# Optimization experiments

Hardware: AMD Instinct MI355X
Metric: run time of the kernel (lower is better)

The kernel has to match this reference:

```python
import jax, jax.numpy as jnp
import numpy as np

T_IN, T_OUT = 16, 25          # in_length, out_length
B, K = 4096, 32               # heroes, neighbors per hero
N = B * K                     # total neighbor tracks
ENC, DEC, DYN, EMB = 64, 128, 32, 32


def _lrelu(x):
    return jnp.where(x >= 0, x, 0.1 * x)


def _lstm(x, Wih, Whh, bih, bhh, hidden):
    """PyTorch-convention LSTM (gate order i,f,g,o). x: [T, B, D]. Returns (all_h [T,B,H], last_h [B,H])."""
    z = jnp.zeros((x.shape[1], hidden), x.dtype)

    def step(carry, xt):
        h, c = carry
        g = xt @ Wih.T + bih + h @ Whh.T + bhh
        i, f, gg, o = jnp.split(g, 4, axis=-1)
        c = jax.nn.sigmoid(f) * c + jax.nn.sigmoid(i) * jnp.tanh(gg)
        h = jax.nn.sigmoid(o) * jnp.tanh(c)
        return (h, c), h

    (h, c), hs = jax.lax.scan(step, (z, z), x)
    return hs, h


def setup_inputs() -> dict:
    key = jax.random.key(0)
    ks = jax.random.split(key, 20)
    p = lambda k, s: jax.random.normal(k, s, jnp.float32) * 0.1
    return {
        "hist": jax.random.normal(ks[0], (T_IN, B, 2), jnp.float32),
        "nbrs": jax.random.normal(ks[1], (T_IN, N, 2), jnp.float32),
        "Wip": p(ks[2], (EMB, 2)), "bip": p(ks[3], (EMB,)),
        "Wih_e": p(ks[4], (4 * ENC, EMB)), "Whh_e": p(ks[5], (4 * ENC, ENC)),
        "bih_e": p(ks[6], (4 * ENC,)), "bhh_e": p(ks[7], (4 * ENC,)),
        "Wdyn": p(ks[8], (DYN, ENC)), "bdyn": p(ks[9], (DYN,)),
        "Wnbr": p(ks[10], (ENC, 2 * T_IN)), "bnbr": p(ks[11], (ENC,)),
        "Wih_d": p(ks[12], (4 * DEC, 2 * DYN)), "Whh_d": p(ks[13], (4 * DEC, DEC)),
        "bih_d": p(ks[14], (4 * DEC,)), "bhh_d": p(ks[15], (4 * DEC,)),
        "Wop": p(ks[16], (2, DEC)), "bop": p(ks[17], (2,)),
        # index_division flattened: neighbor j belongs to hero segment_ids[j] (sorted, K per hero)
        "segment_ids": jnp.repeat(jnp.arange(B, dtype=jnp.int32), K),
    }


def reference(hist, nbrs, Wip, bip, Wih_e, Whh_e, bih_e, bhh_e, Wdyn, bdyn,
              Wnbr, bnbr, Wih_d, Whh_d, bih_d, bhh_d, Wop, bop, segment_ids):
    # --- encode ego history ---
    emb = _lrelu(hist @ Wip.T + bip)                       # [T,B,EMB]
    _, h_enc = _lstm(emb, Wih_e, Whh_e, bih_e, bhh_e, ENC)  # [B,ENC]
    hist_e = _lrelu(h_enc @ Wdyn.T + bdyn)                 # [B,DYN]

    # --- relative neighbor tracks + ragged segment-max pooling ---
    relative = hist[:, segment_ids, :] - nbrs              # [T,N,2]  (hero_repeated gather)
    rela = jnp.transpose(relative, (1, 0, 2)).reshape(N, 2 * T_IN)  # permute(1,0,2).view(-1,2*in_length)
    rela_enc = _lrelu(rela @ Wnbr.T + bnbr)                # [N,ENC]
    scene = jax.ops.segment_max(rela_enc, segment_ids, num_segments=B)  # fused per-group max
    scene = _lrelu(scene @ Wdyn.T + bdyn)                  # [B,DYN]

    # --- decode ---
    enc = jnp.concatenate([hist_e, scene], axis=1)         # [B,2*DYN]
    dec_in = jnp.broadcast_to(enc, (T_OUT, B, 2 * DYN))    # unsqueeze(0).repeat(out_length,1,1)
    h_dec, _ = _lstm(dec_in, Wih_d, Whh_d, bih_d, bhh_d, DEC)  # [T_OUT,B,DEC]
    fut = h_dec @ Wop.T + bop                              # [T_OUT,B,2]
    # outputActivation: with 2 output dims (muX,muY only) it is the identity
    return fut
```

## Files before the change

kernel.cpp:

```cpp
#include <hip/hip_runtime.h>
#include <hip/hip_bf16.h>

#define T_IN   16
#define T_OUT  25
#define BHERO  4096
#define K_NBR  32
#define N_NBR  (BHERO * K_NBR)
#define ENC    64
#define DEC    128
#define DYN    32
#define EMB    32

#define EROW   104
#define DROW   136
#define RROW   40
#define SLABE  (16 * EROW * 2)
#define SLABD  (16 * DROW * 2)

#define OFF_RELA   56576
#define OFF_PMAX   97536
#define OFF_ENC    113152
#define OFF_WOP    117504
#define OFF_WIP    118528
#define OFF_BIP    118784
#define OFF_BOP    118912
#define LDS_TOTAL  118928

typedef __attribute__((ext_vector_type(8))) short bf16x8;
typedef __attribute__((ext_vector_type(4))) float f32x4;

__device__ __forceinline__ float lrelu(float x) { return x >= 0.f ? x : 0.1f * x; }
__device__ __forceinline__ float rcpf(float x)  { return __builtin_amdgcn_rcpf(x); }
__device__ __forceinline__ float sigm(float x)  { return rcpf(1.f + __expf(-x)); }
__device__ __forceinline__ float tanhv(float x) {
    return fmaf(2.f, rcpf(1.f + __expf(-2.f * x)), -1.f);
}
__device__ __forceinline__ short f2bf(float x) {
    __hip_bfloat16 b = __float2bfloat16(x);
    short s; __builtin_memcpy(&s, &b, 2); return s;
}
__device__ __forceinline__ unsigned pk2(float lo, float hi) {
    __hip_bfloat162 p = __float22bfloat162_rn(make_float2(lo, hi));
    unsigned u; __builtin_memcpy(&u, &p, 4); return u;
}
__device__ __forceinline__ bf16x8 mk_frag(float4 f0, float4 f1) {
    uint4 v = { pk2(f0.x, f0.y), pk2(f0.z, f0.w), pk2(f1.x, f1.y), pk2(f1.z, f1.w) };
    bf16x8 r; __builtin_memcpy(&r, &v, 16); return r;
}
__device__ __forceinline__ float bf2f(short s) {
    return __uint_as_float(((unsigned)(unsigned short)s) << 16);
}

__global__ __launch_bounds__(512, 2) void highway_fused(
    const float* __restrict__ hist,  const float* __restrict__ nbrs,
    const float* __restrict__ Wip,   const float* __restrict__ bip,
    const float* __restrict__ WihE,  const float* __restrict__ WhhE,
    const float* __restrict__ bihE,  const float* __restrict__ bhhE,
    const float* __restrict__ Wdyn,  const float* __restrict__ bdyn,
    const float* __restrict__ Wnbr,  const float* __restrict__ bnbr,
    const float* __restrict__ WihD,  const float* __restrict__ WhhD,
    const float* __restrict__ bihD,  const float* __restrict__ bhhD,
    const float* __restrict__ Wop,   const float* __restrict__ bop,
    const int*   __restrict__ seg,
    float* __restrict__ fut)
{
    __shared__ __align__(16) char lds_raw[LDS_TOTAL];
    auto slab   = (short (*)[16][EROW])  lds_raw;
    auto rela   = (short (*)[RROW])     (lds_raw + OFF_RELA);
    auto pmax   = (float (*)[ENC])      (lds_raw + OFF_PMAX);
    auto hist_s = (short (*)[16][DROW])  lds_raw;
    auto enc_s  = (float (*)[68])       (lds_raw + OFF_ENC);
    auto wop_s  = (float (*)[DEC])      (lds_raw + OFF_WOP);
    auto wip_s  = (float (*)[2])        (lds_raw + OFF_WIP);
    auto bip_s  = (float*)              (lds_raw + OFF_BIP);
    auto bop_s  = (float*)              (lds_raw + OFF_BOP);

    const int b0  = blockIdx.x * 16;
    const int n0  = blockIdx.x * 512;
    const int tid = threadIdx.x;
    const int w = tid >> 6, l = tid & 63, r = l & 15, lg = l >> 4;
    const int u0 = w * 16;

    if (tid < EMB) {
        wip_s[tid][0] = Wip[2 * tid];
        wip_s[tid][1] = Wip[2 * tid + 1];
        bip_s[tid]    = bip[tid];
    }
    if (tid < 2 * DEC) wop_s[tid >> 7][tid & 127] = Wop[tid];
    if (tid < 2)       bop_s[tid] = bop[tid];
    for (int i = tid; i < 16 * ENC; i += 512) slab[0][i >> 6][32 + (i & 63)] = 0;

    bf16x8 BfD[4][4];
    float  biasjD[4];
    #pragma unroll
    for (int j = 0; j < 4; ++j) {
        const int col = j * DEC + u0 + r;
        biasjD[j] = bihD[col] + bhhD[col];
        #pragma unroll
        for (int c = 0; c < 4; ++c) {
            const float* src = WhhD + (size_t)col * DEC + c * 32 + 8 * lg;
            BfD[j][c] = mk_frag(*(const float4*)src, *(const float4*)(src + 4));
        }
    }

    bf16x8 BfE[4][3];
    float  biasjE[4];
    bf16x8 BfN[2];
    float  biasn[2];
    if (tid < 256) {
        #pragma unroll
        for (int j = 0; j < 4; ++j) {
            const int col = j * ENC + u0 + r;
            biasjE[j] = bihE[col] + bhhE[col];
            #pragma unroll
            for (int c = 0; c < 3; ++c) {
                const float* src = (c == 0) ? (WihE + (size_t)col * EMB + 8 * lg)
                                            : (WhhE + (size_t)col * ENC + (c - 1) * 32 + 8 * lg);
                BfE[j][c] = mk_frag(*(const float4*)src, *(const float4*)(src + 4));
            }
        }
    } else {
        const int i = w - 4;
        const int ct0 = (i & 1) * 2;
        #pragma unroll
        for (int cc2 = 0; cc2 < 2; ++cc2) {
            const int col = (ct0 + cc2) * 16 + r;
            biasn[cc2] = bnbr[col];
            const float* src = Wnbr + (size_t)col * (2 * T_IN) + 8 * lg;
            BfN[cc2] = mk_frag(*(const float4*)src, *(const float4*)(src + 4));
        }
    }
    __syncthreads();

    if (tid < 256) {
        const int t = tid >> 4, m = tid & 15;
        float2 hv = *(const float2*)&hist[((size_t)t * BHERO + b0 + m) * 2];
        #pragma unroll
        for (int jb = 0; jb < 4; ++jb) {
            float e[8];
            #pragma unroll
            for (int q = 0; q < 8; ++q) {
                int j = jb * 8 + q;
                e[q] = lrelu(hv.x * wip_s[j][0] + hv.y * wip_s[j][1] + bip_s[j]);
            }
            uint4 v = { pk2(e[0],e[1]), pk2(e[2],e[3]), pk2(e[4],e[5]), pk2(e[6],e[7]) };
            __builtin_memcpy(&slab[t][m][jb * 8], &v, 16);
        }
    } else {
        const int x = tid - 256;
        const int n  = x & 31;
        const int ts = x >> 5;
        const int hb = seg[n0 + n];
        float2 h0 = *(const float2*)&hist[((size_t)ts * BHERO + hb) * 2];
        float2 v0 = *(const float2*)&nbrs[((size_t)ts * N_NBR + n0 + n) * 2];
        float2 h1 = *(const float2*)&hist[((size_t)(ts + 8) * BHERO + hb) * 2];
        float2 v1 = *(const float2*)&nbrs[((size_t)(ts + 8) * N_NBR + n0 + n) * 2];
        unsigned* dst = (unsigned*)&rela[n][0];
        dst[ts]     = pk2(h0.x - v0.x, h0.y - v0.y);
        dst[ts + 8] = pk2(h1.x - v1.x, h1.y - v1.y);
    }
    f32x4 cstE = {0.f, 0.f, 0.f, 0.f};
    __syncthreads();

    {
        const char* rbase = lds_raw + (size_t)r * (EROW * 2);
        char*       wbase = lds_raw + SLABE + (size_t)(4 * lg) * (EROW * 2) + (size_t)(32 + u0 + r) * 2;
        const int   x = tid - 256;
        #pragma unroll 1
        for (int t = 0; t < T_IN; ++t) {
            if (tid < 256) {
                const short* rp = (const short*)rbase;
                bf16x8 a0 = *(const bf16x8*)(rp + (0 + lg) * 8);
                bf16x8 a1 = *(const bf16x8*)(rp + (4 + lg) * 8);
                bf16x8 a2 = *(const bf16x8*)(rp + (8 + lg) * 8);
                f32x4 acc[4];
                #pragma unroll
                for (int j = 0; j < 4; ++j) {
                    acc[j] = (f32x4){biasjE[j], biasjE[j], biasjE[j], biasjE[j]};
                    acc[j] = __builtin_amdgcn_mfma_f32_16x16x32_bf16(a0, BfE[j][0], acc[j], 0, 0, 0);
                    acc[j] = __builtin_amdgcn_mfma_f32_16x16x32_bf16(a1, BfE[j][1], acc[j], 0, 0, 0);
                    acc[j] = __builtin_amdgcn_mfma_f32_16x16x32_bf16(a2, BfE[j][2], acc[j], 0, 0, 0);
                }
                float hq[4];
                #pragma unroll
                for (int q = 0; q < 4; ++q) {
                    float ii = sigm(acc[0][q]);
                    float ff = sigm(acc[1][q]);
                    float gg = tanhv(acc[2][q]);
                    float oo = sigm(acc[3][q]);
                    float cc = fmaf(ff, cstE[q], ii * gg);
                    cstE[q] = cc;
                    hq[q] = oo * tanhv(cc);
                }
                unsigned u01 = pk2(hq[0], hq[1]), u23 = pk2(hq[2], hq[3]);
                short* wp = (short*)wbase;
                wp[0 * EROW] = (short)u01; wp[1 * EROW] = (short)(u01 >> 16);
                wp[2 * EROW] = (short)u23; wp[3 * EROW] = (short)(u23 >> 16);
            } else {
                if (t < T_IN - 1) {
                    const int n  = 32 * (t + 1) + (x & 31);
                    const int ts = x >> 5;
                    const int hb = seg[n0 + n];
                    float2 h0 = *(const float2*)&hist[((size_t)ts * BHERO + hb) * 2];
                    float2 v0 = *(const float2*)&nbrs[((size_t)ts * N_NBR + n0 + n) * 2];
                    float2 h1 = *(const float2*)&hist[((size_t)(ts + 8) * BHERO + hb) * 2];
                    float2 v1 = *(const float2*)&nbrs[((size_t)(ts + 8) * N_NBR + n0 + n) * 2];
                    unsigned* dst = (unsigned*)&rela[n][0];
                    dst[ts]     = pk2(h0.x - v0.x, h0.y - v0.y);
                    dst[ts + 8] = pk2(h1.x - v1.x, h1.y - v1.y);
                }
                const int i  = w - 4;
                const int rt = 2 * t + (i >> 1);
                const int ct0 = (i & 1) * 2;
                bf16x8 a = *(const bf16x8*)&rela[rt * 16 + r][8 * lg];
                #pragma unroll
                for (int cc2 = 0; cc2 < 2; ++cc2) {
                    f32x4 acc = {biasn[cc2], biasn[cc2], biasn[cc2], biasn[cc2]};
                    acc = __builtin_amdgcn_mfma_f32_16x16x32_bf16(a, BfN[cc2], acc, 0, 0, 0);
                    float m4 = fmaxf(fmaxf(acc[0], acc[1]), fmaxf(acc[2], acc[3]));
                    m4 = fmaxf(m4, __shfl_xor(m4, 16));
                    m4 = fmaxf(m4, __shfl_xor(m4, 32));
                    if (l < 16) pmax[rt][(ct0 + cc2) * 16 + r] = m4;
                }
            }
            __syncthreads();
            rbase += SLABE; wbase += SLABE;
        }
    }

    #pragma unroll
    for (int it = 0; it < 2; ++it) {
        const int s = tid + 512 * it;
        const int m = s >> 6, col = s & 63;
        const float* wd = Wdyn + (size_t)(col & 31) * ENC;
        float a = bdyn[col & 31];
        if (col < 32) {
            const short* hp = &slab[T_IN][m][32];
            #pragma unroll 8
            for (int k = 0; k < ENC; ++k) a = fmaf(bf2f(hp[k]), wd[k], a);
        } else {
            #pragma unroll 8
            for (int k = 0; k < ENC; ++k) {
                float sv = lrelu(fmaxf(pmax[2 * m][k], pmax[2 * m + 1][k]));
                a = fmaf(sv, wd[k], a);
            }
        }
        enc_s[m][col] = lrelu(a);
    }
    for (int i = tid; i < 16 * DROW; i += 512) ((short*)hist_s)[i] = 0;
    __syncthreads();

    f32x4 xwf[4];
    {
        bf16x8 aE[2];
        #pragma unroll
        for (int c = 0; c < 2; ++c) {
            float4 f0 = *(const float4*)&enc_s[r][c * 32 + 8 * lg];
            float4 f1 = *(const float4*)&enc_s[r][c * 32 + 8 * lg + 4];
            aE[c] = mk_frag(f0, f1);
        }
        #pragma unroll
        for (int j = 0; j < 4; ++j) {
            const int col = j * DEC + u0 + r;
            f32x4 a = {biasjD[j], biasjD[j], biasjD[j], biasjD[j]};
            #pragma unroll
            for (int c = 0; c < 2; ++c) {
                const float* src = WihD + (size_t)col * (2 * DYN) + c * 32 + 8 * lg;
                a = __builtin_amdgcn_mfma_f32_16x16x32_bf16(
                        aE[c], mk_frag(*(const float4*)src, *(const float4*)(src + 4)), a, 0, 0, 0);
            }
            xwf[j] = a;
        }
    }

    f32x4 cst = {0.f, 0.f, 0.f, 0.f};
    {
        const char* rbase = lds_raw + (size_t)r * (DROW * 2);
        char*       wbase = lds_raw + SLABD + (size_t)(4 * lg) * (DROW * 2) + (size_t)(u0 + r) * 2;
        #pragma unroll 1
        for (int t = 0; t < T_OUT; ++t) {
            const short* rp = (const short*)rbase;
            bf16x8 a_[4];
            #pragma unroll
            for (int c = 0; c < 4; ++c)
                a_[c] = *(const bf16x8*)(rp + (4 * c + lg) * 8);
            f32x4 acc[4];
            #pragma unroll
            for (int j = 0; j < 4; ++j) {
                acc[j] = xwf[j];
                #pragma unroll
                for (int c = 0; c < 4; ++c)
                    acc[j] = __builtin_amdgcn_mfma_f32_16x16x32_bf16(a_[c], BfD[j][c], acc[j], 0, 0, 0);
            }
            float hq[4];
            #pragma unroll
            for (int q = 0; q < 4; ++q) {
                float ii = sigm(acc[0][q]);
                float ff = sigm(acc[1][q]);
                float gg = tanhv(acc[2][q]);
                float oo = sigm(acc[3][q]);
                float cc = fmaf(ff, cst[q], ii * gg);
                cst[q] = cc;
                hq[q] = oo * tanhv(cc);
            }
            unsigned u01 = pk2(hq[0], hq[1]), u23 = pk2(hq[2], hq[3]);
            short* wp = (short*)wbase;
            wp[0 * DROW] = (short)u01; wp[1 * DROW] = (short)(u01 >> 16);
            wp[2 * DROW] = (short)u23; wp[3 * DROW] = (short)(u23 >> 16);
            __syncthreads();
            rbase += SLABD; wbase += SLABD;
        }
    }

    if (tid < T_OUT * 16) {
        const int t = tid >> 4, m = tid & 15;
        const short* hp = &hist_s[t + 1][m][0];
        float o0 = bop_s[0], o1 = bop_s[1];
        #pragma unroll
        for (int ub = 0; ub < DEC / 8; ++ub) {
            bf16x8 hv = *(const bf16x8*)(hp + ub * 8);
            #pragma unroll
            for (int e = 0; e < 8; ++e) {
                float h = bf2f(hv[e]);
                o0 = fmaf(h, wop_s[0][ub * 8 + e], o0);
                o1 = fmaf(h, wop_s[1][ub * 8 + e], o1);
            }
        }
        *(float2*)(fut + ((size_t)t * BHERO + b0 + m) * 2) = make_float2(o0, o1);
    }
}

extern "C" void kernel_launch(void* const* d_in, const int* in_sizes, int n_in,
                              void* d_out, int out_size, void* d_ws, size_t ws_size,
                              hipStream_t stream) {
    (void)d_ws; (void)ws_size; (void)in_sizes; (void)n_in; (void)out_size;
    const float* hist  = (const float*)d_in[0];
    const float* nbrs  = (const float*)d_in[1];
    const float* Wip   = (const float*)d_in[2];
    const float* bip   = (const float*)d_in[3];
    const float* Wih_e = (const float*)d_in[4];
    const float* Whh_e = (const float*)d_in[5];
    const float* bih_e = (const float*)d_in[6];
    const float* bhh_e = (const float*)d_in[7];
    const float* Wdyn  = (const float*)d_in[8];
    const float* bdyn  = (const float*)d_in[9];
    const float* Wnbr  = (const float*)d_in[10];
    const float* bnbr  = (const float*)d_in[11];
    const float* Wih_d = (const float*)d_in[12];
    const float* Whh_d = (const float*)d_in[13];
    const float* bih_d = (const float*)d_in[14];
    const float* bhh_d = (const float*)d_in[15];
    const float* Wop   = (const float*)d_in[16];
    const float* bop   = (const float*)d_in[17];
    const int*   seg   = (const int*)d_in[18];
    float* fut = (float*)d_out;

    hipLaunchKernelGGL(highway_fused, dim3(BHERO / 16), dim3(512), 0, stream,
                       hist, nbrs, Wip, bip, Wih_e, Whh_e, bih_e, bhh_e, Wdyn, bdyn,
                       Wnbr, bnbr, Wih_d, Whh_d, bih_d, bhh_d, Wop, bop, seg, fut);
}
```

Measured before the change: 67.04 us.

## Halve heroes per block to 8 and raise occupancy to 4 blocks per CU

```diff
diff --git a/kernel.cpp b/kernel.cpp
--- a/kernel.cpp
+++ b/kernel.cpp
@@ -10,21 +10,22 @@
 #define DEC    128
 #define DYN    32
 #define EMB    32
+#define HEROES 8
 
 #define EROW   104
 #define DROW   136
 #define RROW   40
-#define SLABE  (16 * EROW * 2)
-#define SLABD  (16 * DROW * 2)
-
-#define OFF_RELA   56576
-#define OFF_PMAX   97536
-#define OFF_ENC    113152
-#define OFF_WOP    117504
-#define OFF_WIP    118528
-#define OFF_BIP    118784
-#define OFF_BOP    118912
-#define LDS_TOTAL  118928
+#define SLABE  (HEROES * EROW)
+#define SLABD  (HEROES * DROW)
+
+#define OFF_RELA   28288
+#define OFF_PMAX   48768
+#define OFF_ENC    56576
+#define OFF_WOP    58752
+#define OFF_WIP    59776
+#define OFF_BIP    60032
+#define OFF_BOP    60160
+#define LDS_TOTAL  60176
 
 typedef __attribute__((ext_vector_type(8))) short bf16x8;
 typedef __attribute__((ext_vector_type(4))) float f32x4;
@@ -51,7 +52,7 @@
     return __uint_as_float(((unsigned)(unsigned short)s) << 16);
 }
 
-__global__ __launch_bounds__(512, 2) void highway_fused(
+__global__ __launch_bounds__(512, 4) void highway_fused(
     const float* __restrict__ hist,  const float* __restrict__ nbrs,
     const float* __restrict__ Wip,   const float* __restrict__ bip,
     const float* __restrict__ WihE,  const float* __restrict__ WhhE,
@@ -65,21 +66,24 @@
     float* __restrict__ fut)
 {
     __shared__ __align__(16) char lds_raw[LDS_TOTAL];
-    auto slab   = (short (*)[16][EROW])  lds_raw;
-    auto rela   = (short (*)[RROW])     (lds_raw + OFF_RELA);
-    auto pmax   = (float (*)[ENC])      (lds_raw + OFF_PMAX);
-    auto hist_s = (short (*)[16][DROW])  lds_raw;
-    auto enc_s  = (float (*)[68])       (lds_raw + OFF_ENC);
-    auto wop_s  = (float (*)[DEC])      (lds_raw + OFF_WOP);
-    auto wip_s  = (float (*)[2])        (lds_raw + OFF_WIP);
-    auto bip_s  = (float*)              (lds_raw + OFF_BIP);
-    auto bop_s  = (float*)              (lds_raw + OFF_BOP);
-
-    const int b0  = blockIdx.x * 16;
-    const int n0  = blockIdx.x * 512;
+    auto slab   = (short (*)[HEROES][EROW])  lds_raw;
+    auto rela   = (short (*)[RROW])         (lds_raw + OFF_RELA);
+    auto pmax   = (float (*)[ENC])          (lds_raw + OFF_PMAX);
+    auto hist_s = (short (*)[HEROES][DROW])  lds_raw;
+    auto enc_s  = (float (*)[68])           (lds_raw + OFF_ENC);
+    auto wop_s  = (float (*)[DEC])          (lds_raw + OFF_WOP);
+    auto wip_s  = (float (*)[2])            (lds_raw + OFF_WIP);
+    auto bip_s  = (float*)                  (lds_raw + OFF_BIP);
+    auto bop_s  = (float*)                  (lds_raw + OFF_BOP);
+
+    const int b0  = blockIdx.x * HEROES;
+    const int n0  = blockIdx.x * (HEROES * K_NBR);
     const int tid = threadIdx.x;
     const int w = tid >> 6, l = tid & 63, r = l & 15, lg = l >> 4;
     const int u0 = w * 16;
+    const int r8 = r & 7;
+    const bool lowhalf = (l < 32);
+    const int row0 = lowhalf ? (4 * lg) : (4 * (lg - 2) + 2);
 
     if (tid < EMB) {
         wip_s[tid][0] = Wip[2 * tid];
@@ -88,25 +92,12 @@
     }
     if (tid < 2 * DEC) wop_s[tid >> 7][tid & 127] = Wop[tid];
     if (tid < 2)       bop_s[tid] = bop[tid];
-    for (int i = tid; i < 16 * ENC; i += 512) slab[0][i >> 6][32 + (i & 63)] = 0;
-
-    bf16x8 BfD[4][4];
-    float  biasjD[4];
-    #pragma unroll
-    for (int j = 0; j < 4; ++j) {
-        const int col = j * DEC + u0 + r;
-        biasjD[j] = bihD[col] + bhhD[col];
-        #pragma unroll
-        for (int c = 0; c < 4; ++c) {
-            const float* src = WhhD + (size_t)col * DEC + c * 32 + 8 * lg;
-            BfD[j][c] = mk_frag(*(const float4*)src, *(const float4*)(src + 4));
-        }
-    }
+    slab[0][tid >> 6][32 + (tid & 63)] = 0;
 
     bf16x8 BfE[4][3];
     float  biasjE[4];
-    bf16x8 BfN[2];
-    float  biasn[2];
+    bf16x8 BfN;
+    float  biasn = 0.f;
     if (tid < 256) {
         #pragma unroll
         for (int j = 0; j < 4; ++j) {
@@ -120,56 +111,49 @@
             }
         }
     } else {
-        const int i = w - 4;
-        const int ct0 = (i & 1) * 2;
-        #pragma unroll
-        for (int cc2 = 0; cc2 < 2; ++cc2) {
-            const int col = (ct0 + cc2) * 16 + r;
-            biasn[cc2] = bnbr[col];
-            const float* src = Wnbr + (size_t)col * (2 * T_IN) + 8 * lg;
-            BfN[cc2] = mk_frag(*(const float4*)src, *(const float4*)(src + 4));
-        }
+        const int ct  = w - 4;
+        const int col = ct * 16 + r;
+        biasn = bnbr[col];
+        const float* src = Wnbr + (size_t)col * (2 * T_IN) + 8 * lg;
+        BfN = mk_frag(*(const float4*)src, *(const float4*)(src + 4));
     }
     __syncthreads();
 
     if (tid < 256) {
-        const int t = tid >> 4, m = tid & 15;
+        const int task = tid >> 1;
+        const int t = task >> 3, m = task & 7;
+        const int c0 = (tid & 1) * 16;
         float2 hv = *(const float2*)&hist[((size_t)t * BHERO + b0 + m) * 2];
         #pragma unroll
-        for (int jb = 0; jb < 4; ++jb) {
+        for (int jb = 0; jb < 2; ++jb) {
             float e[8];
             #pragma unroll
             for (int q = 0; q < 8; ++q) {
-                int j = jb * 8 + q;
+                int j = c0 + jb * 8 + q;
                 e[q] = lrelu(hv.x * wip_s[j][0] + hv.y * wip_s[j][1] + bip_s[j]);
             }
             uint4 v = { pk2(e[0],e[1]), pk2(e[2],e[3]), pk2(e[4],e[5]), pk2(e[6],e[7]) };
-            __builtin_memcpy(&slab[t][m][jb * 8], &v, 16);
+            __builtin_memcpy(&slab[t][m][c0 + jb * 8], &v, 16);
         }
     } else {
-        const int x = tid - 256;
-        const int n  = x & 31;
-        const int ts = x >> 5;
+        const int x  = tid - 256;
+        const int n  = x & 15;
+        const int ts = x >> 4;
         const int hb = seg[n0 + n];
-        float2 h0 = *(const float2*)&hist[((size_t)ts * BHERO + hb) * 2];
-        float2 v0 = *(const float2*)&nbrs[((size_t)ts * N_NBR + n0 + n) * 2];
-        float2 h1 = *(const float2*)&hist[((size_t)(ts + 8) * BHERO + hb) * 2];
-        float2 v1 = *(const float2*)&nbrs[((size_t)(ts + 8) * N_NBR + n0 + n) * 2];
-        unsigned* dst = (unsigned*)&rela[n][0];
-        dst[ts]     = pk2(h0.x - v0.x, h0.y - v0.y);
-        dst[ts + 8] = pk2(h1.x - v1.x, h1.y - v1.y);
-    }
-    f32x4 cstE = {0.f, 0.f, 0.f, 0.f};
+        float2 hv = *(const float2*)&hist[((size_t)ts * BHERO + hb) * 2];
+        float2 nv = *(const float2*)&nbrs[((size_t)ts * N_NBR + n0 + n) * 2];
+        ((unsigned*)&rela[n][0])[ts] = pk2(hv.x - nv.x, hv.y - nv.y);
+    }
+    float cE0 = 0.f, cE1 = 0.f;
     __syncthreads();
 
     {
-        const char* rbase = lds_raw + (size_t)r * (EROW * 2);
-        char*       wbase = lds_raw + SLABE + (size_t)(4 * lg) * (EROW * 2) + (size_t)(32 + u0 + r) * 2;
-        const int   x = tid - 256;
+        const short* rp = (const short*)lds_raw + r8 * EROW;
+        short*       wp = (short*)lds_raw + SLABE + row0 * EROW + (32 + u0 + r);
+        const int    x  = tid - 256;
         #pragma unroll 1
         for (int t = 0; t < T_IN; ++t) {
             if (tid < 256) {
-                const short* rp = (const short*)rbase;
                 bf16x8 a0 = *(const bf16x8*)(rp + (0 + lg) * 8);
                 bf16x8 a1 = *(const bf16x8*)(rp + (4 + lg) * 8);
                 bf16x8 a2 = *(const bf16x8*)(rp + (8 + lg) * 8);
@@ -181,57 +165,45 @@
                     acc[j] = __builtin_amdgcn_mfma_f32_16x16x32_bf16(a1, BfE[j][1], acc[j], 0, 0, 0);
                     acc[j] = __builtin_amdgcn_mfma_f32_16x16x32_bf16(a2, BfE[j][2], acc[j], 0, 0, 0);
                 }
-                float hq[4];
+                float g0[4], g1[4];
                 #pragma unroll
-                for (int q = 0; q < 4; ++q) {
-                    float ii = sigm(acc[0][q]);
-                    float ff = sigm(acc[1][q]);
-                    float gg = tanhv(acc[2][q]);
-                    float oo = sigm(acc[3][q]);
-                    float cc = fmaf(ff, cstE[q], ii * gg);
-                    cstE[q] = cc;
-                    hq[q] = oo * tanhv(cc);
+                for (int j = 0; j < 4; ++j) {
+                    float t2 = __shfl(acc[j][2], l & 31);
+                    float t3 = __shfl(acc[j][3], l & 31);
+                    g0[j] = lowhalf ? acc[j][0] : t2;
+                    g1[j] = lowhalf ? acc[j][1] : t3;
                 }
-                unsigned u01 = pk2(hq[0], hq[1]), u23 = pk2(hq[2], hq[3]);
-                short* wp = (short*)wbase;
-                wp[0 * EROW] = (short)u01; wp[1 * EROW] = (short)(u01 >> 16);
-                wp[2 * EROW] = (short)u23; wp[3 * EROW] = (short)(u23 >> 16);
+                float i0 = sigm(g0[0]), f0 = sigm(g0[1]), G0 = tanhv(g0[2]), o0 = sigm(g0[3]);
+                float i1 = sigm(g1[0]), f1 = sigm(g1[1]), G1 = tanhv(g1[2]), o1 = sigm(g1[3]);
+                cE0 = fmaf(f0, cE0, i0 * G0);
+                cE1 = fmaf(f1, cE1, i1 * G1);
+                unsigned u = pk2(o0 * tanhv(cE0), o1 * tanhv(cE1));
+                wp[0]    = (short)u;
+                wp[EROW] = (short)(u >> 16);
             } else {
                 if (t < T_IN - 1) {
-                    const int n  = 32 * (t + 1) + (x & 31);
-                    const int ts = x >> 5;
+                    const int n  = 16 * (t + 1) + (x & 15);
+                    const int ts = x >> 4;
                     const int hb = seg[n0 + n];
-                    float2 h0 = *(const float2*)&hist[((size_t)ts * BHERO + hb) * 2];
-                    float2 v0 = *(const float2*)&nbrs[((size_t)ts * N_NBR + n0 + n) * 2];
-                    float2 h1 = *(const float2*)&hist[((size_t)(ts + 8) * BHERO + hb) * 2];
-                    float2 v1 = *(const float2*)&nbrs[((size_t)(ts + 8) * N_NBR + n0 + n) * 2];
-                    unsigned* dst = (unsigned*)&rela[n][0];
-                    dst[ts]     = pk2(h0.x - v0.x, h0.y - v0.y);
-                    dst[ts + 8] = pk2(h1.x - v1.x, h1.y - v1.y);
+                    float2 hv = *(const float2*)&hist[((size_t)ts * BHERO + hb) * 2];
+                    float2 nv = *(const float2*)&nbrs[((size_t)ts * N_NBR + n0 + n) * 2];
+                    ((unsigned*)&rela[n][0])[ts] = pk2(hv.x - nv.x, hv.y - nv.y);
                 }
-                const int i  = w - 4;
-                const int rt = 2 * t + (i >> 1);
-                const int ct0 = (i & 1) * 2;
-                bf16x8 a = *(const bf16x8*)&rela[rt * 16 + r][8 * lg];
-                #pragma unroll
-                for (int cc2 = 0; cc2 < 2; ++cc2) {
-                    f32x4 acc = {biasn[cc2], biasn[cc2], biasn[cc2], biasn[cc2]};
-                    acc = __builtin_amdgcn_mfma_f32_16x16x32_bf16(a, BfN[cc2], acc, 0, 0, 0);
-                    float m4 = fmaxf(fmaxf(acc[0], acc[1]), fmaxf(acc[2], acc[3]));
-                    m4 = fmaxf(m4, __shfl_xor(m4, 16));
-                    m4 = fmaxf(m4, __shfl_xor(m4, 32));
-                    if (l < 16) pmax[rt][(ct0 + cc2) * 16 + r] = m4;
-                }
+                bf16x8 a = *(const bf16x8*)&rela[t * 16 + r][8 * lg];
+                f32x4 acc = {biasn, biasn, biasn, biasn};
+                acc = __builtin_amdgcn_mfma_f32_16x16x32_bf16(a, BfN, acc, 0, 0, 0);
+                float m4 = fmaxf(fmaxf(acc[0], acc[1]), fmaxf(acc[2], acc[3]));
+                m4 = fmaxf(m4, __shfl_xor(m4, 16));
+                m4 = fmaxf(m4, __shfl_xor(m4, 32));
+                if (l < 16) pmax[t][(w - 4) * 16 + r] = m4;
             }
             __syncthreads();
-            rbase += SLABE; wbase += SLABE;
-        }
-    }
-
-    #pragma unroll
-    for (int it = 0; it < 2; ++it) {
-        const int s = tid + 512 * it;
-        const int m = s >> 6, col = s & 63;
+            rp += SLABE; wp += SLABE;
+        }
+    }
+
+    {
+        const int m = tid >> 6, col = tid & 63;
         const float* wd = Wdyn + (size_t)(col & 31) * ENC;
         float a = bdyn[col & 31];
         if (col < 32) {
@@ -246,17 +218,29 @@
             }
         }
         enc_s[m][col] = lrelu(a);
-    }
-    for (int i = tid; i < 16 * DROW; i += 512) ((short*)hist_s)[i] = 0;
+        for (int i = tid; i < SLABD; i += 512) ((short*)hist_s)[i] = 0;
+    }
     __syncthreads();
 
+    bf16x8 BfD[4][4];
+    float  biasjD[4];
+    #pragma unroll
+    for (int j = 0; j < 4; ++j) {
+        const int col = j * DEC + u0 + r;
+        biasjD[j] = bihD[col] + bhhD[col];
+        #pragma unroll
+        for (int c = 0; c < 4; ++c) {
+            const float* src = WhhD + (size_t)col * DEC + c * 32 + 8 * lg;
+            BfD[j][c] = mk_frag(*(const float4*)src, *(const float4*)(src + 4));
+        }
+    }
     f32x4 xwf[4];
     {
         bf16x8 aE[2];
         #pragma unroll
         for (int c = 0; c < 2; ++c) {
-            float4 f0 = *(const float4*)&enc_s[r][c * 32 + 8 * lg];
-            float4 f1 = *(const float4*)&enc_s[r][c * 32 + 8 * lg + 4];
+            float4 f0 = *(const float4*)&enc_s[r8][c * 32 + 8 * lg];
+            float4 f1 = *(const float4*)&enc_s[r8][c * 32 + 8 * lg + 4];
             aE[c] = mk_frag(f0, f1);
         }
         #pragma unroll
@@ -273,13 +257,12 @@
         }
     }
 
-    f32x4 cst = {0.f, 0.f, 0.f, 0.f};
+    float c0 = 0.f, c1 = 0.f;
     {
-        const char* rbase = lds_raw + (size_t)r * (DROW * 2);
-        char*       wbase = lds_raw + SLABD + (size_t)(4 * lg) * (DROW * 2) + (size_t)(u0 + r) * 2;
+        const short* rp = (const short*)lds_raw + r8 * DROW;
+        short*       wp = (short*)lds_raw + SLABD + row0 * DROW + (u0 + r);
         #pragma unroll 1
         for (int t = 0; t < T_OUT; ++t) {
-            const short* rp = (const short*)rbase;
             bf16x8 a_[4];
             #pragma unroll
             for (int c = 0; c < 4; ++c)
@@ -292,28 +275,28 @@
                 for (int c = 0; c < 4; ++c)
                     acc[j] = __builtin_amdgcn_mfma_f32_16x16x32_bf16(a_[c], BfD[j][c], acc[j], 0, 0, 0);
             }
-            float hq[4];
-            #pragma unroll
-            for (int q = 0; q < 4; ++q) {
-                float ii = sigm(acc[0][q]);
-                float ff = sigm(acc[1][q]);
-                float gg = tanhv(acc[2][q]);
-                float oo = sigm(acc[3][q]);
-                float cc = fmaf(ff, cst[q], ii * gg);
-                cst[q] = cc;
-                hq[q] = oo * tanhv(cc);
-            }
-            unsigned u01 = pk2(hq[0], hq[1]), u23 = pk2(hq[2], hq[3]);
-            short* wp = (short*)wbase;
-            wp[0 * DROW] = (short)u01; wp[1 * DROW] = (short)(u01 >> 16);
-            wp[2 * DROW] = (short)u23; wp[3 * DROW] = (short)(u23 >> 16);
+            float g0[4], g1[4];
+            #pragma unroll
+            for (int j = 0; j < 4; ++j) {
+                float t2 = __shfl(acc[j][2], l & 31);
+                float t3 = __shfl(acc[j][3], l & 31);
+                g0[j] = lowhalf ? acc[j][0] : t2;
+                g1[j] = lowhalf ? acc[j][1] : t3;
+            }
+            float i0 = sigm(g0[0]), f0 = sigm(g0[1]), G0 = tanhv(g0[2]), o0 = sigm(g0[3]);
+            float i1 = sigm(g1[0]), f1 = sigm(g1[1]), G1 = tanhv(g1[2]), o1 = sigm(g1[3]);
+            c0 = fmaf(f0, c0, i0 * G0);
+            c1 = fmaf(f1, c1, i1 * G1);
+            unsigned u = pk2(o0 * tanhv(c0), o1 * tanhv(c1));
+            wp[0]    = (short)u;
+            wp[DROW] = (short)(u >> 16);
             __syncthreads();
-            rbase += SLABD; wbase += SLABD;
-        }
-    }
-
-    if (tid < T_OUT * 16) {
-        const int t = tid >> 4, m = tid & 15;
+            rp += SLABD; wp += SLABD;
+        }
+    }
+
+    if (tid < T_OUT * HEROES) {
+        const int t = tid >> 3, m = tid & 7;
         const short* hp = &hist_s[t + 1][m][0];
         float o0 = bop_s[0], o1 = bop_s[1];
         #pragma unroll
@@ -355,7 +338,7 @@
     const int*   seg   = (const int*)d_in[18];
     float* fut = (float*)d_out;
 
-    hipLaunchKernelGGL(highway_fused, dim3(BHERO / 16), dim3(512), 0, stream,
+    hipLaunchKernelGGL(highway_fused, dim3(BHERO / HEROES), dim3(512), 0, stream,
                        hist, nbrs, Wip, bip, Wih_e, Whh_e, bih_e, bhh_e, Wdyn, bdyn,
                        Wnbr, bnbr, Wih_d, Whh_d, bih_d, bhh_d, Wop, bop, seg, fut);
 }
```

Measured after the change: 70.26 us. +4.8%, slower.

## Split decoder LSTM gates across 16 waves with LDS gate exchange

Applied to the files above, without the earlier changes.

```diff
diff --git a/kernel.cpp b/kernel.cpp
--- a/kernel.cpp
+++ b/kernel.cpp
@@ -14,17 +14,19 @@
 #define EROW   104
 #define DROW   136
 #define RROW   40
-#define SLABE  (16 * EROW * 2)
-#define SLABD  (16 * DROW * 2)
+#define SLABE_S (16 * EROW)
+#define SLABD_S (16 * DROW)
 
 #define OFF_RELA   56576
 #define OFF_PMAX   97536
-#define OFF_ENC    113152
-#define OFF_WOP    117504
-#define OFF_WIP    118528
-#define OFF_BIP    118784
-#define OFF_BOP    118912
-#define LDS_TOTAL  118928
+#define OFF_BUFA   113152
+#define OFF_BUFB   123392
+#define OFF_ENC    141824
+#define OFF_WOP    146176
+#define OFF_WIP    147200
+#define OFF_BIP    147456
+#define OFF_BOP    147584
+#define LDS_TOTAL  147592
 
 typedef __attribute__((ext_vector_type(8))) short bf16x8;
 typedef __attribute__((ext_vector_type(4))) float f32x4;
@@ -51,7 +53,7 @@
     return __uint_as_float(((unsigned)(unsigned short)s) << 16);
 }
 
-__global__ __launch_bounds__(512, 2) void highway_fused(
+__global__ __launch_bounds__(1024, 4) void highway_fused(
     const float* __restrict__ hist,  const float* __restrict__ nbrs,
     const float* __restrict__ Wip,   const float* __restrict__ bip,
     const float* __restrict__ WihE,  const float* __restrict__ WhhE,
@@ -69,6 +71,8 @@
     auto rela   = (short (*)[RROW])     (lds_raw + OFF_RELA);
     auto pmax   = (float (*)[ENC])      (lds_raw + OFF_PMAX);
     auto hist_s = (short (*)[16][DROW])  lds_raw;
+    auto bufA   = (float (*)[20])       (lds_raw + OFF_BUFA);
+    auto bufB   = (float2 (*)[18])      (lds_raw + OFF_BUFB);
     auto enc_s  = (float (*)[68])       (lds_raw + OFF_ENC);
     auto wop_s  = (float (*)[DEC])      (lds_raw + OFF_WOP);
     auto wip_s  = (float (*)[2])        (lds_raw + OFF_WIP);
@@ -79,7 +83,6 @@
     const int n0  = blockIdx.x * 512;
     const int tid = threadIdx.x;
     const int w = tid >> 6, l = tid & 63, r = l & 15, lg = l >> 4;
-    const int u0 = w * 16;
 
     if (tid < EMB) {
         wip_s[tid][0] = Wip[2 * tid];
@@ -88,30 +91,18 @@
     }
     if (tid < 2 * DEC) wop_s[tid >> 7][tid & 127] = Wop[tid];
     if (tid < 2)       bop_s[tid] = bop[tid];
-    for (int i = tid; i < 16 * ENC; i += 512) slab[0][i >> 6][32 + (i & 63)] = 0;
-
-    bf16x8 BfD[4][4];
-    float  biasjD[4];
-    #pragma unroll
-    for (int j = 0; j < 4; ++j) {
-        const int col = j * DEC + u0 + r;
-        biasjD[j] = bihD[col] + bhhD[col];
-        #pragma unroll
-        for (int c = 0; c < 4; ++c) {
-            const float* src = WhhD + (size_t)col * DEC + c * 32 + 8 * lg;
-            BfD[j][c] = mk_frag(*(const float4*)src, *(const float4*)(src + 4));
-        }
-    }
+    slab[0][tid >> 6][32 + (tid & 63)] = 0;
 
     bf16x8 BfE[4][3];
-    float  biasjE[4];
+    float  biasE[4];
     bf16x8 BfN[2];
-    float  biasn[2];
+    float  biasn[2] = {0.f, 0.f};
     if (tid < 256) {
+        const int u0e = w * 16;
         #pragma unroll
         for (int j = 0; j < 4; ++j) {
-            const int col = j * ENC + u0 + r;
-            biasjE[j] = bihE[col] + bhhE[col];
+            const int col = j * ENC + u0e + r;
+            biasE[j] = bihE[col] + bhhE[col];
             #pragma unroll
             for (int c = 0; c < 3; ++c) {
                 const float* src = (c == 0) ? (WihE + (size_t)col * EMB + 8 * lg)
@@ -119,7 +110,7 @@
                 BfE[j][c] = mk_frag(*(const float4*)src, *(const float4*)(src + 4));
             }
         }
-    } else {
+    } else if (tid < 512) {
         const int i = w - 4;
         const int ct0 = (i & 1) * 2;
         #pragma unroll
@@ -146,8 +137,8 @@
             uint4 v = { pk2(e[0],e[1]), pk2(e[2],e[3]), pk2(e[4],e[5]), pk2(e[6],e[7]) };
             __builtin_memcpy(&slab[t][m][jb * 8], &v, 16);
         }
-    } else {
-        const int x = tid - 256;
+    } else if (tid < 512) {
+        const int x  = tid - 256;
         const int n  = x & 31;
         const int ts = x >> 5;
         const int hb = seg[n0 + n];
@@ -163,20 +154,19 @@
     __syncthreads();
 
     {
-        const char* rbase = lds_raw + (size_t)r * (EROW * 2);
-        char*       wbase = lds_raw + SLABE + (size_t)(4 * lg) * (EROW * 2) + (size_t)(32 + u0 + r) * 2;
-        const int   x = tid - 256;
+        const short* rp  = (const short*)lds_raw + r * EROW;
+        short*       wpE = (short*)lds_raw + SLABE_S + (4 * lg) * EROW + (32 + w * 16 + r);
+        const int    x   = tid - 256;
         #pragma unroll 1
         for (int t = 0; t < T_IN; ++t) {
             if (tid < 256) {
-                const short* rp = (const short*)rbase;
                 bf16x8 a0 = *(const bf16x8*)(rp + (0 + lg) * 8);
                 bf16x8 a1 = *(const bf16x8*)(rp + (4 + lg) * 8);
                 bf16x8 a2 = *(const bf16x8*)(rp + (8 + lg) * 8);
                 f32x4 acc[4];
                 #pragma unroll
                 for (int j = 0; j < 4; ++j) {
-                    acc[j] = (f32x4){biasjE[j], biasjE[j], biasjE[j], biasjE[j]};
+                    acc[j] = (f32x4){biasE[j], biasE[j], biasE[j], biasE[j]};
                     acc[j] = __builtin_amdgcn_mfma_f32_16x16x32_bf16(a0, BfE[j][0], acc[j], 0, 0, 0);
                     acc[j] = __builtin_amdgcn_mfma_f32_16x16x32_bf16(a1, BfE[j][1], acc[j], 0, 0, 0);
                     acc[j] = __builtin_amdgcn_mfma_f32_16x16x32_bf16(a2, BfE[j][2], acc[j], 0, 0, 0);
@@ -193,10 +183,9 @@
                     hq[q] = oo * tanhv(cc);
                 }
                 unsigned u01 = pk2(hq[0], hq[1]), u23 = pk2(hq[2], hq[3]);
-                short* wp = (short*)wbase;
-                wp[0 * EROW] = (short)u01; wp[1 * EROW] = (short)(u01 >> 16);
-                wp[2 * EROW] = (short)u23; wp[3 * EROW] = (short)(u23 >> 16);
-            } else {
+                wpE[0 * EROW] = (short)u01; wpE[1 * EROW] = (short)(u01 >> 16);
+                wpE[2 * EROW] = (short)u23; wpE[3 * EROW] = (short)(u23 >> 16);
+            } else if (tid < 512) {
                 if (t < T_IN - 1) {
                     const int n  = 32 * (t + 1) + (x & 31);
                     const int ts = x >> 5;
@@ -224,14 +213,12 @@
                 }
             }
             __syncthreads();
-            rbase += SLABE; wbase += SLABE;
-        }
-    }
-
-    #pragma unroll
-    for (int it = 0; it < 2; ++it) {
-        const int s = tid + 512 * it;
-        const int m = s >> 6, col = s & 63;
+            rp += SLABE_S; wpE += SLABE_S;
+        }
+    }
+
+    {
+        const int m = tid >> 6, col = tid & 63;
         const float* wd = Wdyn + (size_t)(col & 31) * ENC;
         float a = bdyn[col & 31];
         if (col < 32) {
@@ -246,11 +233,32 @@
             }
         }
         enc_s[m][col] = lrelu(a);
-    }
-    for (int i = tid; i < 16 * DROW; i += 512) ((short*)hist_s)[i] = 0;
+        for (int i = tid; i < SLABD_S; i += 1024) ((short*)hist_s)[i] = 0;
+    }
     __syncthreads();
 
-    f32x4 xwf[4];
+    const bool ig  = (w < 8);
+    const int  ub  = w & 7;
+    const int  u0d = ub * 16;
+    const int  qb  = ig ? 0 : 2;
+    const int  j0  = ig ? 0 : 1;
+    const int  j1  = ig ? 2 : 3;
+    bf16x8 BfD[2][4];
+    float  biasD[2];
+    {
+        const int colA = j0 * DEC + u0d + r;
+        const int colB = j1 * DEC + u0d + r;
+        biasD[0] = bihD[colA] + bhhD[colA];
+        biasD[1] = bihD[colB] + bhhD[colB];
+        #pragma unroll
+        for (int c = 0; c < 4; ++c) {
+            const float* sA = WhhD + (size_t)colA * DEC + c * 32 + 8 * lg;
+            const float* sB = WhhD + (size_t)colB * DEC + c * 32 + 8 * lg;
+            BfD[0][c] = mk_frag(*(const float4*)sA, *(const float4*)(sA + 4));
+            BfD[1][c] = mk_frag(*(const float4*)sB, *(const float4*)(sB + 4));
+        }
+    }
+    f32x4 xwf0, xwf1;
     {
         bf16x8 aE[2];
         #pragma unroll
@@ -259,56 +267,71 @@
             float4 f1 = *(const float4*)&enc_s[r][c * 32 + 8 * lg + 4];
             aE[c] = mk_frag(f0, f1);
         }
-        #pragma unroll
-        for (int j = 0; j < 4; ++j) {
-            const int col = j * DEC + u0 + r;
-            f32x4 a = {biasjD[j], biasjD[j], biasjD[j], biasjD[j]};
-            #pragma unroll
-            for (int c = 0; c < 2; ++c) {
-                const float* src = WihD + (size_t)col * (2 * DYN) + c * 32 + 8 * lg;
-                a = __builtin_amdgcn_mfma_f32_16x16x32_bf16(
-                        aE[c], mk_frag(*(const float4*)src, *(const float4*)(src + 4)), a, 0, 0, 0);
-            }
-            xwf[j] = a;
-        }
-    }
-
-    f32x4 cst = {0.f, 0.f, 0.f, 0.f};
-    {
-        const char* rbase = lds_raw + (size_t)r * (DROW * 2);
-        char*       wbase = lds_raw + SLABD + (size_t)(4 * lg) * (DROW * 2) + (size_t)(u0 + r) * 2;
+        const int colA = j0 * DEC + u0d + r;
+        const int colB = j1 * DEC + u0d + r;
+        xwf0 = (f32x4){biasD[0], biasD[0], biasD[0], biasD[0]};
+        xwf1 = (f32x4){biasD[1], biasD[1], biasD[1], biasD[1]};
+        #pragma unroll
+        for (int c = 0; c < 2; ++c) {
+            const float* sA = WihD + (size_t)colA * (2 * DYN) + c * 32 + 8 * lg;
+            const float* sB = WihD + (size_t)colB * (2 * DYN) + c * 32 + 8 * lg;
+            xwf0 = __builtin_amdgcn_mfma_f32_16x16x32_bf16(
+                       aE[c], mk_frag(*(const float4*)sA, *(const float4*)(sA + 4)), xwf0, 0, 0, 0);
+            xwf1 = __builtin_amdgcn_mfma_f32_16x16x32_bf16(
+                       aE[c], mk_frag(*(const float4*)sB, *(const float4*)(sB + 4)), xwf1, 0, 0, 0);
+        }
+    }
+
+    float c0 = 0.f, c1 = 0.f;
+    {
+        const short* rp = (const short*)lds_raw + r * DROW;
+        short*       wp = (short*)lds_raw + SLABD_S + (4 * lg + qb) * DROW + (u0d + r);
+        float*  bArow = &bufA[u0d + r][0];
+        float2* bBrow = &bufB[u0d + r][0];
         #pragma unroll 1
         for (int t = 0; t < T_OUT; ++t) {
-            const short* rp = (const short*)rbase;
             bf16x8 a_[4];
             #pragma unroll
             for (int c = 0; c < 4; ++c)
                 a_[c] = *(const bf16x8*)(rp + (4 * c + lg) * 8);
-            f32x4 acc[4];
-            #pragma unroll
-            for (int j = 0; j < 4; ++j) {
-                acc[j] = xwf[j];
-                #pragma unroll
-                for (int c = 0; c < 4; ++c)
-                    acc[j] = __builtin_amdgcn_mfma_f32_16x16x32_bf16(a_[c], BfD[j][c], acc[j], 0, 0, 0);
-            }
-            float hq[4];
-            #pragma unroll
-            for (int q = 0; q < 4; ++q) {
-                float ii = sigm(acc[0][q]);
-                float ff = sigm(acc[1][q]);
-                float gg = tanhv(acc[2][q]);
-                float oo = sigm(acc[3][q]);
-                float cc = fmaf(ff, cst[q], ii * gg);
-                cst[q] = cc;
-                hq[q] = oo * tanhv(cc);
-            }
-            unsigned u01 = pk2(hq[0], hq[1]), u23 = pk2(hq[2], hq[3]);
-            short* wp = (short*)wbase;
-            wp[0 * DROW] = (short)u01; wp[1 * DROW] = (short)(u01 >> 16);
-            wp[2 * DROW] = (short)u23; wp[3 * DROW] = (short)(u23 >> 16);
+            f32x4 acc0 = xwf0, acc1 = xwf1;
+            #pragma unroll
+            for (int c = 0; c < 4; ++c) {
+                acc0 = __builtin_amdgcn_mfma_f32_16x16x32_bf16(a_[c], BfD[0][c], acc0, 0, 0, 0);
+                acc1 = __builtin_amdgcn_mfma_f32_16x16x32_bf16(a_[c], BfD[1][c], acc1, 0, 0, 0);
+            }
+            float sA0, sA1, sf0, so0, sf1, so1;
+            if (ig) {
+                float s0 = sigm(acc0[0]) * tanhv(acc1[0]);
+                float s1 = sigm(acc0[1]) * tanhv(acc1[1]);
+                float s2 = sigm(acc0[2]) * tanhv(acc1[2]);
+                float s3 = sigm(acc0[3]) * tanhv(acc1[3]);
+                *(float4*)&bArow[4 * lg] = make_float4(s0, s1, s2, s3);
+                sA0 = s0; sA1 = s1;
+            } else {
+                float f0v = sigm(acc0[0]), o0v = sigm(acc1[0]);
+                float f1v = sigm(acc0[1]), o1v = sigm(acc1[1]);
+                float f2v = sigm(acc0[2]), o2v = sigm(acc1[2]);
+                float f3v = sigm(acc0[3]), o3v = sigm(acc1[3]);
+                *(float4*)&bBrow[4 * lg]     = make_float4(f0v, o0v, f1v, o1v);
+                *(float4*)&bBrow[4 * lg + 2] = make_float4(f2v, o2v, f3v, o3v);
+                sf0 = f2v; so0 = o2v; sf1 = f3v; so1 = o3v;
+            }
             __syncthreads();
-            rbase += SLABD; wbase += SLABD;
+            if (ig) {
+                float4 v = *(const float4*)&bBrow[4 * lg];
+                sf0 = v.x; so0 = v.y; sf1 = v.z; so1 = v.w;
+            } else {
+                float2 sg = *(const float2*)&bArow[4 * lg + 2];
+                sA0 = sg.x; sA1 = sg.y;
+            }
+            c0 = fmaf(sf0, c0, sA0);
+            c1 = fmaf(sf1, c1, sA1);
+            unsigned u = pk2(so0 * tanhv(c0), so1 * tanhv(c1));
+            wp[0]    = (short)u;
+            wp[DROW] = (short)(u >> 16);
+            __syncthreads();
+            rp += SLABD_S; wp += SLABD_S;
         }
     }
 
@@ -317,13 +340,13 @@
         const short* hp = &hist_s[t + 1][m][0];
         float o0 = bop_s[0], o1 = bop_s[1];
         #pragma unroll
-        for (int ub = 0; ub < DEC / 8; ++ub) {
-            bf16x8 hv = *(const bf16x8*)(hp + ub * 8);
+        for (int ubk = 0; ubk < DEC / 8; ++ubk) {
+            bf16x8 hv = *(const bf16x8*)(hp + ubk * 8);
             #pragma unroll
             for (int e = 0; e < 8; ++e) {
                 float h = bf2f(hv[e]);
-                o0 = fmaf(h, wop_s[0][ub * 8 + e], o0);
-                o1 = fmaf(h, wop_s[1][ub * 8 + e], o1);
+                o0 = fmaf(h, wop_s[0][ubk * 8 + e], o0);
+                o1 = fmaf(h, wop_s[1][ubk * 8 + e], o1);
             }
         }
         *(float2*)(fut + ((size_t)t * BHERO + b0 + m) * 2) = make_float2(o0, o1);
@@ -355,7 +378,7 @@
     const int*   seg   = (const int*)d_in[18];
     float* fut = (float*)d_out;
 
-    hipLaunchKernelGGL(highway_fused, dim3(BHERO / 16), dim3(512), 0, stream,
+    hipLaunchKernelGGL(highway_fused, dim3(BHERO / 16), dim3(1024), 0, stream,
                        hist, nbrs, Wip, bip, Wih_e, Whh_e, bih_e, bhh_e, Wdyn, bdyn,
                        Wnbr, bnbr, Wih_d, Whh_d, bih_d, bhh_d, Wop, bop, seg, fut);
 }
```

Measured after the change: 67.56 us. About the same (+0.8%).

## Fold log2e gate scaling into LSTM weights, split MFMA chains, defer decoder weight load

Applied to the files above, without the earlier changes.

```diff
diff --git a/kernel.cpp b/kernel.cpp
--- a/kernel.cpp
+++ b/kernel.cpp
@@ -26,14 +26,18 @@
 #define OFF_BOP    118912
 #define LDS_TOTAL  118928
 
+#define L2E 1.44269504f
+
 typedef __attribute__((ext_vector_type(8))) short bf16x8;
 typedef __attribute__((ext_vector_type(4))) float f32x4;
 
 __device__ __forceinline__ float lrelu(float x) { return x >= 0.f ? x : 0.1f * x; }
 __device__ __forceinline__ float rcpf(float x)  { return __builtin_amdgcn_rcpf(x); }
-__device__ __forceinline__ float sigm(float x)  { return rcpf(1.f + __expf(-x)); }
-__device__ __forceinline__ float tanhv(float x) {
-    return fmaf(2.f, rcpf(1.f + __expf(-2.f * x)), -1.f);
+__device__ __forceinline__ float ex2(float x)   { return __builtin_amdgcn_exp2f(x); }
+__device__ __forceinline__ float sigm2(float x) { return rcpf(1.f + ex2(-x)); }
+__device__ __forceinline__ float tanh2(float x) { return fmaf(2.f, rcpf(1.f + ex2(-x)), -1.f); }
+__device__ __forceinline__ float tanhc(float c) {
+    return fmaf(2.f, rcpf(1.f + ex2(-2.f * L2E * c)), -1.f);
 }
 __device__ __forceinline__ short f2bf(float x) {
     __hip_bfloat16 b = __float2bfloat16(x);
@@ -45,6 +49,10 @@
 }
 __device__ __forceinline__ bf16x8 mk_frag(float4 f0, float4 f1) {
     uint4 v = { pk2(f0.x, f0.y), pk2(f0.z, f0.w), pk2(f1.x, f1.y), pk2(f1.z, f1.w) };
+    bf16x8 r; __builtin_memcpy(&r, &v, 16); return r;
+}
+__device__ __forceinline__ bf16x8 mk_frag_s(float4 f0, float4 f1, float s) {
+    uint4 v = { pk2(f0.x*s, f0.y*s), pk2(f0.z*s, f0.w*s), pk2(f1.x*s, f1.y*s), pk2(f1.z*s, f1.w*s) };
     bf16x8 r; __builtin_memcpy(&r, &v, 16); return r;
 }
 __device__ __forceinline__ float bf2f(short s) {
@@ -79,7 +87,6 @@
     const int n0  = blockIdx.x * 512;
     const int tid = threadIdx.x;
     const int w = tid >> 6, l = tid & 63, r = l & 15, lg = l >> 4;
-    const int u0 = w * 16;
 
     if (tid < EMB) {
         wip_s[tid][0] = Wip[2 * tid];
@@ -90,33 +97,21 @@
     if (tid < 2)       bop_s[tid] = bop[tid];
     for (int i = tid; i < 16 * ENC; i += 512) slab[0][i >> 6][32 + (i & 63)] = 0;
 
-    bf16x8 BfD[4][4];
-    float  biasjD[4];
-    #pragma unroll
-    for (int j = 0; j < 4; ++j) {
-        const int col = j * DEC + u0 + r;
-        biasjD[j] = bihD[col] + bhhD[col];
-        #pragma unroll
-        for (int c = 0; c < 4; ++c) {
-            const float* src = WhhD + (size_t)col * DEC + c * 32 + 8 * lg;
-            BfD[j][c] = mk_frag(*(const float4*)src, *(const float4*)(src + 4));
-        }
-    }
-
     bf16x8 BfE[4][3];
-    float  biasjE[4];
+    float  biasE[4];
     bf16x8 BfN[2];
-    float  biasn[2];
+    float  biasn[2] = {0.f, 0.f};
     if (tid < 256) {
         #pragma unroll
         for (int j = 0; j < 4; ++j) {
-            const int col = j * ENC + u0 + r;
-            biasjE[j] = bihE[col] + bhhE[col];
+            const float sj  = (j == 2) ? (2.f * L2E) : L2E;
+            const int   col = j * ENC + w * 16 + r;
+            biasE[j] = (bihE[col] + bhhE[col]) * sj;
             #pragma unroll
             for (int c = 0; c < 3; ++c) {
                 const float* src = (c == 0) ? (WihE + (size_t)col * EMB + 8 * lg)
                                             : (WhhE + (size_t)col * ENC + (c - 1) * 32 + 8 * lg);
-                BfE[j][c] = mk_frag(*(const float4*)src, *(const float4*)(src + 4));
+                BfE[j][c] = mk_frag_s(*(const float4*)src, *(const float4*)(src + 4), sj);
             }
         }
     } else {
@@ -164,7 +159,7 @@
 
     {
         const char* rbase = lds_raw + (size_t)r * (EROW * 2);
-        char*       wbase = lds_raw + SLABE + (size_t)(4 * lg) * (EROW * 2) + (size_t)(32 + u0 + r) * 2;
+        char*       wbase = lds_raw + SLABE + (size_t)(4 * lg) * (EROW * 2) + (size_t)(32 + w * 16 + r) * 2;
         const int   x = tid - 256;
         #pragma unroll 1
         for (int t = 0; t < T_IN; ++t) {
@@ -176,21 +171,23 @@
                 f32x4 acc[4];
                 #pragma unroll
                 for (int j = 0; j < 4; ++j) {
-                    acc[j] = (f32x4){biasjE[j], biasjE[j], biasjE[j], biasjE[j]};
-                    acc[j] = __builtin_amdgcn_mfma_f32_16x16x32_bf16(a0, BfE[j][0], acc[j], 0, 0, 0);
-                    acc[j] = __builtin_amdgcn_mfma_f32_16x16x32_bf16(a1, BfE[j][1], acc[j], 0, 0, 0);
-                    acc[j] = __builtin_amdgcn_mfma_f32_16x16x32_bf16(a2, BfE[j][2], acc[j], 0, 0, 0);
+                    f32x4 aA = (f32x4){biasE[j], biasE[j], biasE[j], biasE[j]};
+                    f32x4 aB = (f32x4){0.f, 0.f, 0.f, 0.f};
+                    aA = __builtin_amdgcn_mfma_f32_16x16x32_bf16(a0, BfE[j][0], aA, 0, 0, 0);
+                    aB = __builtin_amdgcn_mfma_f32_16x16x32_bf16(a1, BfE[j][1], aB, 0, 0, 0);
+                    aA = __builtin_amdgcn_mfma_f32_16x16x32_bf16(a2, BfE[j][2], aA, 0, 0, 0);
+                    acc[j] = aA + aB;
                 }
                 float hq[4];
                 #pragma unroll
                 for (int q = 0; q < 4; ++q) {
-                    float ii = sigm(acc[0][q]);
-                    float ff = sigm(acc[1][q]);
-                    float gg = tanhv(acc[2][q]);
-                    float oo = sigm(acc[3][q]);
+                    float ii = sigm2(acc[0][q]);
+                    float ff = sigm2(acc[1][q]);
+                    float gg = tanh2(acc[2][q]);
+                    float oo = sigm2(acc[3][q]);
                     float cc = fmaf(ff, cstE[q], ii * gg);
                     cstE[q] = cc;
-                    hq[q] = oo * tanhv(cc);
+                    hq[q] = oo * tanhc(cc);
                 }
                 unsigned u01 = pk2(hq[0], hq[1]), u23 = pk2(hq[2], hq[3]);
                 short* wp = (short*)wbase;
@@ -236,13 +233,22 @@
         float a = bdyn[col & 31];
         if (col < 32) {
             const short* hp = &slab[T_IN][m][32];
-            #pragma unroll 8
-            for (int k = 0; k < ENC; ++k) a = fmaf(bf2f(hp[k]), wd[k], a);
+            #pragma unroll
+            for (int kb = 0; kb < 8; ++kb) {
+                bf16x8 hv = *(const bf16x8*)(hp + kb * 8);
+                #pragma unroll
+                for (int e = 0; e < 8; ++e)
+                    a = fmaf(bf2f(hv[e]), wd[kb * 8 + e], a);
+            }
         } else {
-            #pragma unroll 8
-            for (int k = 0; k < ENC; ++k) {
-                float sv = lrelu(fmaxf(pmax[2 * m][k], pmax[2 * m + 1][k]));
-                a = fmaf(sv, wd[k], a);
+            #pragma unroll
+            for (int kb = 0; kb < 16; ++kb) {
+                float4 p0 = *(const float4*)&pmax[2 * m][kb * 4];
+                float4 p1 = *(const float4*)&pmax[2 * m + 1][kb * 4];
+                a = fmaf(lrelu(fmaxf(p0.x, p1.x)), wd[kb * 4 + 0], a);
+                a = fmaf(lrelu(fmaxf(p0.y, p1.y)), wd[kb * 4 + 1], a);
+                a = fmaf(lrelu(fmaxf(p0.z, p1.z)), wd[kb * 4 + 2], a);
+                a = fmaf(lrelu(fmaxf(p0.w, p1.w)), wd[kb * 4 + 3], a);
             }
         }
         enc_s[m][col] = lrelu(a);
@@ -250,6 +256,22 @@
     for (int i = tid; i < 16 * DROW; i += 512) ((short*)hist_s)[i] = 0;
     __syncthreads();
 
+    const int u0 = w * 16;
+    bf16x8 BfD[4][4];
+    float  biasD[4];
+    float  sjD[4];
+    #pragma unroll
+    for (int j = 0; j < 4; ++j) {
+        const float sj  = (j == 2) ? (2.f * L2E) : L2E;
+        const int   col = j * DEC + u0 + r;
+        sjD[j]   = sj;
+        biasD[j] = (bihD[col] + bhhD[col]) * sj;
+        #pragma unroll
+        for (int c = 0; c < 4; ++c) {
+            const float* src = WhhD + (size_t)col * DEC + c * 32 + 8 * lg;
+            BfD[j][c] = mk_frag_s(*(const float4*)src, *(const float4*)(src + 4), sj);
+        }
+    }
     f32x4 xwf[4];
     {
         bf16x8 aE[2];
@@ -262,12 +284,13 @@
         #pragma unroll
         for (int j = 0; j < 4; ++j) {
             const int col = j * DEC + u0 + r;
-            f32x4 a = {biasjD[j], biasjD[j], biasjD[j], biasjD[j]};
+            f32x4 a = {biasD[j], biasD[j], biasD[j], biasD[j]};
             #pragma unroll
             for (int c = 0; c < 2; ++c) {
                 const float* src = WihD + (size_t)col * (2 * DYN) + c * 32 + 8 * lg;
                 a = __builtin_amdgcn_mfma_f32_16x16x32_bf16(
-                        aE[c], mk_frag(*(const float4*)src, *(const float4*)(src + 4)), a, 0, 0, 0);
+                        aE[c], mk_frag_s(*(const float4*)src, *(const float4*)(src + 4), sjD[j]),
+                        a, 0, 0, 0);
             }
             xwf[j] = a;
         }
@@ -287,21 +310,24 @@
             f32x4 acc[4];
             #pragma unroll
             for (int j = 0; j < 4; ++j) {
-                acc[j] = xwf[j];
-                #pragma unroll
-                for (int c = 0; c < 4; ++c)
-                    acc[j] = __builtin_amdgcn_mfma_f32_16x16x32_bf16(a_[c], BfD[j][c], acc[j], 0, 0, 0);
+                f32x4 aA = xwf[j];
+                f32x4 aB = (f32x4){0.f, 0.f, 0.f, 0.f};
+                aA = __builtin_amdgcn_mfma_f32_16x16x32_bf16(a_[0], BfD[j][0], aA, 0, 0, 0);
+                aB = __builtin_amdgcn_mfma_f32_16x16x32_bf16(a_[1], BfD[j][1], aB, 0, 0, 0);
+                aA = __builtin_amdgcn_mfma_f32_16x16x32_bf16(a_[2], BfD[j][2], aA, 0, 0, 0);
+                aB = __builtin_amdgcn_mfma_f32_16x16x32_bf16(a_[3], BfD[j][3], aB, 0, 0, 0);
+                acc[j] = aA + aB;
             }
             float hq[4];
             #pragma unroll
             for (int q = 0; q < 4; ++q) {
-                float ii = sigm(acc[0][q]);
-                float ff = sigm(acc[1][q]);
-                float gg = tanhv(acc[2][q]);
-                float oo = sigm(acc[3][q]);
+                float ii = sigm2(acc[0][q]);
+                float ff = sigm2(acc[1][q]);
+                float gg = tanh2(acc[2][q]);
+                float oo = sigm2(acc[3][q]);
                 float cc = fmaf(ff, cst[q], ii * gg);
                 cst[q] = cc;
-                hq[q] = oo * tanhv(cc);
+                hq[q] = oo * tanhc(cc);
             }
             unsigned u01 = pk2(hq[0], hq[1]), u23 = pk2(hq[2], hq[3]);
             short* wp = (short*)wbase;
```

After: 63.58 us. -5.2%, faster.
